# Performance work log

Measured on AMD Instinct MI355X. Metric: run time of the kernel, lower is better.

The kernel has to match this reference:

```python
import jax, jax.numpy as jnp
import numpy as np

N_QUBITS = 14
N_LAYERS = 4
N_CLASSES = 10
BATCH = 1024


def apply_1q(state, gate, wire):
    """Apply a 2x2 gate ([2,2] shared or [B,2,2] batched) to `wire` of state [B,2,...,2]."""
    s = jnp.moveaxis(state, wire + 1, -1)
    shp = s.shape
    s = s.reshape(shp[0], -1, 2)
    if gate.ndim == 3:
        s = jnp.einsum('bij,bkj->bki', gate, s)
    else:
        s = jnp.einsum('ij,bkj->bki', gate, s)
    return jnp.moveaxis(s.reshape(shp), -1, wire + 1)


def apply_cnot(state, c, t):
    s = jnp.moveaxis(state, (c + 1, t + 1), (-2, -1))
    s = jnp.stack([s[..., 0, :], s[..., 1, ::-1]], axis=-2)
    return jnp.moveaxis(s, (-2, -1), (c + 1, t + 1))


def simulate(x, q_params):
    """Batched statevector sim of: RY(x_i) embed -> BasicEntanglerLayers(RX + CNOT ring) -> <Z_i>."""
    B, n = x.shape
    state = jnp.zeros((B,) + (2,) * n, jnp.complex64)
    state = state.at[(slice(None),) + (0,) * n].set(1.0)

    # RY(x_i) on each wire (angles batched per sample)
    c, s = jnp.cos(0.5 * x), jnp.sin(0.5 * x)
    for w in range(n):
        g = jnp.stack([jnp.stack([c[:, w], -s[:, w]], -1),
                       jnp.stack([s[:, w], c[:, w]], -1)], -2).astype(jnp.complex64)  # [B,2,2]
        state = apply_1q(state, g, w)

    # BasicEntanglerLayers: per layer RX(weights[l,i]) on every wire, then CNOT ring
    cw, sw = jnp.cos(0.5 * q_params), jnp.sin(0.5 * q_params)
    n_layers = q_params.shape[0]
    for l in range(n_layers):
        for w in range(n):
            cc = cw[l, w].astype(jnp.complex64)
            isw = (-1j) * sw[l, w].astype(jnp.complex64)
            g = jnp.stack([jnp.stack([cc, isw]), jnp.stack([isw, cc])])  # [2,2] RX
            state = apply_1q(state, g, w)
        if n == 2:
            state = apply_cnot(state, 0, 1)
        else:
            for w in range(n):
                state = apply_cnot(state, w, (w + 1) % n)

    # <Z_i> = P(bit_i=0) - P(bit_i=1)
    p = jnp.abs(state) ** 2  # [B,2,...,2] real
    axes_all = tuple(range(1, n + 1))
    z = []
    for w in range(n):
        pw = jnp.sum(p, axis=tuple(a for a in axes_all if a != w + 1))  # [B,2]
        z.append(pw[:, 0] - pw[:, 1])
    return jnp.stack(z, -1).astype(jnp.float32)  # [B, n]


def setup_inputs() -> dict:
    key = jax.random.key(0)
    k1, k2, k3, k4 = jax.random.split(key, 4)
    x = jax.random.normal(k1, (BATCH, N_QUBITS), dtype=jnp.float32)
    q_params = 0.01 * jax.random.normal(k2, (N_LAYERS, N_QUBITS), dtype=jnp.float32)
    fc_w = jax.random.normal(k3, (N_CLASSES, N_QUBITS), dtype=jnp.float32) / np.sqrt(N_QUBITS)
    fc_b = jax.random.normal(k4, (N_CLASSES,), dtype=jnp.float32) * 0.01
    return {"x": x, "q_params": q_params, "fc_w": fc_w, "fc_b": fc_b}


def reference(x, q_params, fc_w, fc_b):
    q_out = simulate(x, q_params)            # [B, n_qubits]
    logits = q_out @ fc_w.T + fc_b           # [B, n_classes]
    return logits
```

## Files before the change

kernel.cpp:

```cpp
#include <hip/hip_runtime.h>
#include <hip/hip_fp16.h>
#include <math.h>


#define NQ 14
#define NSTATE (1 << NQ)
#define NLAYERS 4
#define NCLASSES 10
#define BLOCK 512
#define PADN (NSTATE + (NSTATE >> 5))

template<int LO, int M, int STEP, bool IS_RX, bool INIT, int PRE_CTRL, int POST_CTRL, bool CHAIN, bool FINAL>
__device__ __forceinline__ void run_pass(__half2* __restrict__ st,
                                         const __half2* __restrict__ cw,
                                         const __half2* __restrict__ sw,
                                         float* __restrict__ zloc)
{
  constexpr int KN  = 1 << M;
  constexpr int NCH = NSTATE >> M;
  __half2 c[M], s[M];
#pragma unroll
  for (int j = 0; j < M; ++j) { c[j] = cw[j]; s[j] = sw[j]; }

  for (int chunk = threadIdx.x; chunk < NCH; chunk += BLOCK) {
    const int low   = chunk & ((1 << LO) - 1);
    const int high  = chunk >> LO;
    const int base  = low | (high << (LO + M));
    const int pbase = base + (base >> 5);
    __half2 a[KN];
    if constexpr (INIT) {
#pragma unroll
      for (int k = 0; k < KN; ++k) a[k] = __floats2half2_rn(0.f, 0.f);
      if (chunk == 0) a[0] = __floats2half2_rn(1.f, 0.f);
    } else {
#pragma unroll
      for (int k = 0; k < KN; ++k) a[k] = st[pbase + k * STEP];
    }
    if constexpr (PRE_CTRL >= 0) {
      if ((base >> PRE_CTRL) & 1) {
#pragma unroll
        for (int k = 0; k < KN; k += 2) { __half2 t = a[k]; a[k] = a[k + 1]; a[k + 1] = t; }
      }
    }
#pragma unroll
    for (int j = 0; j < M; ++j) {
#pragma unroll
      for (int k = 0; k < KN; ++k) {
        if ((k & (1 << j)) == 0) {
          const int k1 = k | (1 << j);
          const __half2 a0 = a[k], a1 = a[k1];
          if constexpr (IS_RX) {
            a[k]  = __hfma2(s[j], __lowhigh2highlow(a1), __hmul2(c[j], a0));
            a[k1] = __hfma2(s[j], __lowhigh2highlow(a0), __hmul2(c[j], a1));
          } else {
            a[k]  = __hsub2(__hmul2(c[j], a0), __hmul2(s[j], a1));
            a[k1] = __hfma2(s[j], a0, __hmul2(c[j], a1));
          }
        }
      }
    }
    if constexpr (POST_CTRL >= 0) {
      if ((base >> POST_CTRL) & 1) {
#pragma unroll
        for (int k = 0; k < KN; k += 2) { __half2 t = a[k]; a[k] = a[k + 1]; a[k + 1] = t; }
      }
    }
    if constexpr (CHAIN) {
#pragma unroll
      for (int j = 0; j < M - 1; ++j) {
#pragma unroll
        for (int k = 0; k < KN; ++k) {
          if ((k & (1 << j)) != 0 && (k & (1 << (j + 1))) == 0) {
            const int k2 = k | (1 << (j + 1));
            __half2 t = a[k]; a[k] = a[k2]; a[k2] = t;
          }
        }
      }
    }
    if constexpr (FINAL) {
      float ssum = 0.f, sb0 = 0.f, sb1 = 0.f, sb2 = 0.f, sb3 = 0.f;
#pragma unroll
      for (int k = 0; k < KN; ++k) {
        const float2 v = __half22float2(a[k]);
        const float p = fmaf(v.x, v.x, v.y * v.y);
        ssum += p;
        if (k & 1) sb0 += p;
        if (k & 2) sb1 += p;
        if (k & 4) sb2 += p;
        if (k & 8) sb3 += p;
      }
      zloc[10] += ssum - 2.f * sb0;
      zloc[11] += ssum - 2.f * sb1;
      zloc[12] += ssum - 2.f * sb2;
      zloc[13] += ssum - 2.f * sb3;
      const float z0 = ssum - 2.f * sb3;
      zloc[0] += (base & 1) ? -z0 : z0;
#pragma unroll
      for (int w = 1; w < 10; ++w) zloc[w] += ((base >> w) & 1) ? -ssum : ssum;
    } else {
#pragma unroll
      for (int k = 0; k < KN; ++k) st[pbase + k * STEP] = a[k];
    }
  }
}

__global__ __launch_bounds__(BLOCK) void qsim_kernel(
    const float* __restrict__ x, const float* __restrict__ qp,
    const float* __restrict__ fcw, const float* __restrict__ fcb,
    float* __restrict__ out)
{
  extern __shared__ unsigned char smem[];
  __half2* st  = (__half2*)smem;
  __half2* ryc = st + PADN;
  __half2* rys = ryc + NQ;
  __half2* rxc = rys + NQ;
  __half2* rxs = rxc + NLAYERS * NQ;
  float*   zbuf  = (float*)(rxs + NLAYERS * NQ);
  float*   zpart = zbuf + NQ;

  const int b   = blockIdx.x;
  const int tid = threadIdx.x;

  if (tid < NQ) {
    float sv, cv;
    sincosf(0.5f * x[b * NQ + tid], &sv, &cv);
    ryc[tid] = __floats2half2_rn(cv, cv);
    rys[tid] = __floats2half2_rn(sv, sv);
  } else if (tid >= 64 && tid < 64 + NLAYERS * NQ) {
    const int k = tid - 64;
    float sv, cv;
    sincosf(0.5f * qp[k], &sv, &cv);
    rxc[k] = __floats2half2_rn(cv, cv);
    rxs[k] = __floats2half2_rn(sv, -sv);
  }
  __syncthreads();

  run_pass<0, 5, 1,    false, true,  -1, -1, false, false>(st, ryc,      rys,      nullptr); __syncthreads();
  run_pass<5, 5, 33,   false, false, -1, -1, false, false>(st, ryc + 5,  rys + 5,  nullptr); __syncthreads();
  run_pass<10, 4, 1056,false, false, -1, -1, false, false>(st, ryc + 10, rys + 10, nullptr); __syncthreads();

  float zloc[NQ];
#pragma unroll
  for (int w = 0; w < NQ; ++w) zloc[w] = 0.f;

#pragma unroll
  for (int l = 0; l < NLAYERS; ++l) {
    const __half2* lc = rxc + l * NQ;
    const __half2* ls = rxs + l * NQ;
    if (l == 0) run_pass<0, 5, 1, true, false, -1, -1, true, false>(st, lc, ls, nullptr);
    else        run_pass<0, 5, 1, true, false, 13, -1, true, false>(st, lc, ls, nullptr);
    __syncthreads();
    run_pass<5, 5, 33, true, false, -1, 4, true, false>(st, lc + 5, ls + 5, nullptr);
    __syncthreads();
    if (l < NLAYERS - 1) {
      run_pass<10, 4, 1056, true, false, -1, 9, true, false>(st, lc + 10, ls + 10, nullptr);
      __syncthreads();
    } else {
      run_pass<10, 4, 1056, true, false, -1, 9, true, true>(st, lc + 10, ls + 10, zloc);
    }
  }

#pragma unroll
  for (int w = 0; w < NQ; ++w) {
#pragma unroll
    for (int off = 32; off > 0; off >>= 1)
      zloc[w] += __shfl_down(zloc[w], off, 64);
  }
  const int wave = tid >> 6, lane = tid & 63;
  if (lane == 0) {
#pragma unroll
    for (int w = 0; w < NQ; ++w) zpart[wave * NQ + w] = zloc[w];
  }
  __syncthreads();
  if (tid < NQ) {
    float acc = 0.f;
#pragma unroll
    for (int v = 0; v < BLOCK / 64; ++v) acc += zpart[v * NQ + tid];
    zbuf[tid] = acc;
  }
  __syncthreads();

  if (tid < NCLASSES) {
    float acc = fcb[tid];
#pragma unroll
    for (int w = 0; w < NQ; ++w) acc = fmaf(zbuf[w], fcw[tid * NQ + w], acc);
    out[b * NCLASSES + tid] = acc;
  }
}

extern "C" void kernel_launch(void* const* d_in, const int* in_sizes, int n_in,
                              void* d_out, int out_size, void* d_ws, size_t ws_size,
                              hipStream_t stream) {
  const float* x   = (const float*)d_in[0];
  const float* qp  = (const float*)d_in[1];
  const float* fcw = (const float*)d_in[2];
  const float* fcb = (const float*)d_in[3];
  float* out = (float*)d_out;
  const int B = in_sizes[0] / NQ;

  const size_t shmem = (size_t)PADN * sizeof(__half2)
                     + (size_t)(2 * NQ + 2 * NLAYERS * NQ) * sizeof(__half2)
                     + (size_t)(NQ + (BLOCK / 64) * NQ) * sizeof(float);
  (void)hipFuncSetAttribute((const void*)qsim_kernel,
                            hipFuncAttributeMaxDynamicSharedMemorySize, (int)shmem);
  qsim_kernel<<<B, BLOCK, shmem, stream>>>(x, qp, fcw, fcb, out);
}
```

Measured before the change: 145.2 us.

## Restructure state passes for vectorized LDS access with wider padding

Replaces the generic templated pass with three specialized passes (A, B, C) that read and write shared-memory state using float4/float2 vector loads. The padding now inserts 4 half2 words every 32 instead of one, so 8- and 16-byte accesses stay aligned. Pass B gives each thread two adjacent amplitudes per group and runs on only 256 threads with 64 amplitudes each. The aim is fewer, wider LDS instructions with fewer bank conflicts, at the cost of higher register pressure and half the threads idle in pass B.

```diff
diff --git a/kernel.cpp b/kernel.cpp
--- a/kernel.cpp
+++ b/kernel.cpp
@@ -4,102 +4,193 @@
 
 
 #define NQ 14
-#define NSTATE (1 << NQ)
+#define NSTATE 16384
 #define NLAYERS 4
 #define NCLASSES 10
 #define BLOCK 512
-#define PADN (NSTATE + (NSTATE >> 5))
-
-template<int LO, int M, int STEP, bool IS_RX, bool INIT, int PRE_CTRL, int POST_CTRL, bool CHAIN, bool FINAL>
-__device__ __forceinline__ void run_pass(__half2* __restrict__ st,
-                                         const __half2* __restrict__ cw,
-                                         const __half2* __restrict__ sw,
-                                         float* __restrict__ zloc)
-{
-  constexpr int KN  = 1 << M;
-  constexpr int NCH = NSTATE >> M;
-  __half2 c[M], s[M];
-#pragma unroll
-  for (int j = 0; j < M; ++j) { c[j] = cw[j]; s[j] = sw[j]; }
-
-  for (int chunk = threadIdx.x; chunk < NCH; chunk += BLOCK) {
-    const int low   = chunk & ((1 << LO) - 1);
-    const int high  = chunk >> LO;
-    const int base  = low | (high << (LO + M));
-    const int pbase = base + (base >> 5);
-    __half2 a[KN];
-    if constexpr (INIT) {
-#pragma unroll
-      for (int k = 0; k < KN; ++k) a[k] = __floats2half2_rn(0.f, 0.f);
-      if (chunk == 0) a[0] = __floats2half2_rn(1.f, 0.f);
-    } else {
-#pragma unroll
-      for (int k = 0; k < KN; ++k) a[k] = st[pbase + k * STEP];
-    }
-    if constexpr (PRE_CTRL >= 0) {
-      if ((base >> PRE_CTRL) & 1) {
-#pragma unroll
-        for (int k = 0; k < KN; k += 2) { __half2 t = a[k]; a[k] = a[k + 1]; a[k + 1] = t; }
-      }
-    }
-#pragma unroll
-    for (int j = 0; j < M; ++j) {
-#pragma unroll
-      for (int k = 0; k < KN; ++k) {
-        if ((k & (1 << j)) == 0) {
-          const int k1 = k | (1 << j);
-          const __half2 a0 = a[k], a1 = a[k1];
-          if constexpr (IS_RX) {
-            a[k]  = __hfma2(s[j], __lowhigh2highlow(a1), __hmul2(c[j], a0));
-            a[k1] = __hfma2(s[j], __lowhigh2highlow(a0), __hmul2(c[j], a1));
-          } else {
-            a[k]  = __hsub2(__hmul2(c[j], a0), __hmul2(s[j], a1));
-            a[k1] = __hfma2(s[j], a0, __hmul2(c[j], a1));
-          }
+#define PADN (NSTATE + ((NSTATE >> 5) << 2))
+
+__device__ __forceinline__ int pidx(int i) { return i + ((i >> 5) << 2); }
+__device__ __forceinline__ __half2 f2h(float f) { return __builtin_bit_cast(__half2, f); }
+__device__ __forceinline__ float   h2f(__half2 h) { return __builtin_bit_cast(float, h); }
+
+template<bool IS_RX>
+__device__ __forceinline__ void rot_pair(__half2& a0r, __half2& a1r,
+                                         const __half2 cj, const __half2 sj,
+                                         const __half2 nsj)
+{
+  const __half2 a0 = a0r, a1 = a1r;
+  if constexpr (IS_RX) {
+    a0r = __hfma2(sj, __lowhigh2highlow(a1), __hmul2(cj, a0));
+    a1r = __hfma2(sj, __lowhigh2highlow(a0), __hmul2(cj, a1));
+  } else {
+    a0r = __hfma2(nsj, a1, __hmul2(cj, a0));
+    a1r = __hfma2(sj,  a0, __hmul2(cj, a1));
+  }
+}
+
+template<bool IS_RX, bool INIT, bool PRE_WRAP, bool CHAIN>
+__device__ __forceinline__ void pass_A(__half2* __restrict__ st,
+                                       const __half2* __restrict__ cw,
+                                       const __half2* __restrict__ sw)
+{
+  __half2 c[5], s[5];
+#pragma unroll
+  for (int j = 0; j < 5; ++j) { c[j] = cw[j]; s[j] = sw[j]; }
+  const int ch = threadIdx.x;
+  float4* base = (float4*)(st + 36 * ch);
+  __half2 a[32];
+  if constexpr (INIT) {
+#pragma unroll
+    for (int k = 0; k < 32; ++k) a[k] = f2h(0.f);
+    if (ch == 0) a[0] = __floats2half2_rn(1.f, 0.f);
+  } else {
+#pragma unroll
+    for (int m = 0; m < 8; ++m) {
+      const float4 v = base[m];
+      a[4*m+0] = f2h(v.x); a[4*m+1] = f2h(v.y);
+      a[4*m+2] = f2h(v.z); a[4*m+3] = f2h(v.w);
+    }
+  }
+  if constexpr (PRE_WRAP) {
+    if ((ch >> 8) & 1) {
+#pragma unroll
+      for (int k = 0; k < 32; k += 2) { __half2 t = a[k]; a[k] = a[k+1]; a[k+1] = t; }
+    }
+  }
+#pragma unroll
+  for (int j = 0; j < 5; ++j) {
+    const __half2 cj = c[j], sj = s[j], nsj = __hneg2(s[j]);
+#pragma unroll
+    for (int k = 0; k < 32; ++k)
+      if ((k & (1 << j)) == 0) rot_pair<IS_RX>(a[k], a[k | (1 << j)], cj, sj, nsj);
+  }
+  if constexpr (CHAIN) {
+#pragma unroll
+    for (int j = 0; j < 4; ++j)
+#pragma unroll
+      for (int k = 0; k < 32; ++k)
+        if ((k & (1 << j)) != 0 && (k & (2 << j)) == 0) {
+          const int k2 = k | (2 << j);
+          __half2 t = a[k]; a[k] = a[k2]; a[k2] = t;
         }
-      }
-    }
-    if constexpr (POST_CTRL >= 0) {
-      if ((base >> POST_CTRL) & 1) {
-#pragma unroll
-        for (int k = 0; k < KN; k += 2) { __half2 t = a[k]; a[k] = a[k + 1]; a[k + 1] = t; }
-      }
-    }
-    if constexpr (CHAIN) {
-#pragma unroll
-      for (int j = 0; j < M - 1; ++j) {
-#pragma unroll
-        for (int k = 0; k < KN; ++k) {
-          if ((k & (1 << j)) != 0 && (k & (1 << (j + 1))) == 0) {
-            const int k2 = k | (1 << (j + 1));
-            __half2 t = a[k]; a[k] = a[k2]; a[k2] = t;
-          }
+  }
+#pragma unroll
+  for (int m = 0; m < 8; ++m) {
+    float4 v;
+    v.x = h2f(a[4*m+0]); v.y = h2f(a[4*m+1]);
+    v.z = h2f(a[4*m+2]); v.w = h2f(a[4*m+3]);
+    base[m] = v;
+  }
+}
+
+template<bool IS_RX, bool DO_CNOT>
+__device__ __forceinline__ void pass_B(__half2* __restrict__ st,
+                                       const __half2* __restrict__ cw,
+                                       const __half2* __restrict__ sw)
+{
+  __half2 c[5], s[5];
+#pragma unroll
+  for (int j = 0; j < 5; ++j) { c[j] = cw[j]; s[j] = sw[j]; }
+  const int ch = threadIdx.x;
+  __half2* bp = st + pidx(((ch & 15) << 1) | ((ch >> 4) << 10));
+  __half2 a[64];
+#pragma unroll
+  for (int g = 0; g < 32; ++g) {
+    const float2 v = *(const float2*)(bp + 36 * g);
+    a[2*g] = f2h(v.x); a[2*g+1] = f2h(v.y);
+  }
+#pragma unroll
+  for (int j = 0; j < 5; ++j) {
+    const __half2 cj = c[j], sj = s[j], nsj = __hneg2(s[j]);
+#pragma unroll
+    for (int r = 0; r < 64; ++r)
+      if ((r & (2 << j)) == 0) rot_pair<IS_RX>(a[r], a[r | (2 << j)], cj, sj, nsj);
+  }
+  if constexpr (DO_CNOT) {
+    if ((ch >> 3) & 1) {
+#pragma unroll
+      for (int r = 0; r < 64; ++r)
+        if ((r & 2) == 0) { const int r1 = r | 2; __half2 t = a[r]; a[r] = a[r1]; a[r1] = t; }
+    }
+#pragma unroll
+    for (int j = 0; j < 4; ++j)
+#pragma unroll
+      for (int r = 0; r < 64; ++r)
+        if ((r & (2 << j)) != 0 && (r & (4 << j)) == 0) {
+          const int r2 = r | (4 << j);
+          __half2 t = a[r]; a[r] = a[r2]; a[r2] = t;
         }
-      }
-    }
-    if constexpr (FINAL) {
-      float ssum = 0.f, sb0 = 0.f, sb1 = 0.f, sb2 = 0.f, sb3 = 0.f;
-#pragma unroll
-      for (int k = 0; k < KN; ++k) {
-        const float2 v = __half22float2(a[k]);
-        const float p = fmaf(v.x, v.x, v.y * v.y);
-        ssum += p;
-        if (k & 1) sb0 += p;
-        if (k & 2) sb1 += p;
-        if (k & 4) sb2 += p;
-        if (k & 8) sb3 += p;
-      }
-      zloc[10] += ssum - 2.f * sb0;
-      zloc[11] += ssum - 2.f * sb1;
-      zloc[12] += ssum - 2.f * sb2;
-      zloc[13] += ssum - 2.f * sb3;
-      const float z0 = ssum - 2.f * sb3;
-      zloc[0] += (base & 1) ? -z0 : z0;
-#pragma unroll
-      for (int w = 1; w < 10; ++w) zloc[w] += ((base >> w) & 1) ? -ssum : ssum;
-    } else {
-#pragma unroll
-      for (int k = 0; k < KN; ++k) st[pbase + k * STEP] = a[k];
+  }
+#pragma unroll
+  for (int g = 0; g < 32; ++g) {
+    float2 v; v.x = h2f(a[2*g]); v.y = h2f(a[2*g+1]);
+    *(float2*)(bp + 36 * g) = v;
+  }
+}
+
+template<bool IS_RX, bool DO_CNOT, bool FINAL>
+__device__ __forceinline__ void pass_C(__half2* __restrict__ st,
+                                       const __half2* __restrict__ cw,
+                                       const __half2* __restrict__ sw,
+                                       float* __restrict__ zloc)
+{
+  __half2 c[4], s[4];
+#pragma unroll
+  for (int j = 0; j < 4; ++j) { c[j] = cw[j]; s[j] = sw[j]; }
+  const int ch = threadIdx.x;
+  __half2* bp = st + pidx(ch << 1);
+  __half2 a[32];
+#pragma unroll
+  for (int h = 0; h < 16; ++h) {
+    const float2 v = *(const float2*)(bp + 1152 * h);
+    a[2*h] = f2h(v.x); a[2*h+1] = f2h(v.y);
+  }
+#pragma unroll
+  for (int j = 0; j < 4; ++j) {
+    const __half2 cj = c[j], sj = s[j], nsj = __hneg2(s[j]);
+#pragma unroll
+    for (int r = 0; r < 32; ++r)
+      if ((r & (2 << j)) == 0) rot_pair<IS_RX>(a[r], a[r | (2 << j)], cj, sj, nsj);
+  }
+  if constexpr (DO_CNOT) {
+    if ((ch >> 8) & 1) {
+#pragma unroll
+      for (int r = 0; r < 32; ++r)
+        if ((r & 2) == 0) { const int r1 = r | 2; __half2 t = a[r]; a[r] = a[r1]; a[r1] = t; }
+    }
+#pragma unroll
+    for (int j = 0; j < 3; ++j)
+#pragma unroll
+      for (int r = 0; r < 32; ++r)
+        if ((r & (2 << j)) != 0 && (r & (4 << j)) == 0) {
+          const int r2 = r | (4 << j);
+          __half2 t = a[r]; a[r] = a[r2]; a[r2] = t;
+        }
+  }
+  if constexpr (FINAL) {
+    float ssum = 0.f, sx0 = 0.f, sb[4] = {0.f, 0.f, 0.f, 0.f};
+#pragma unroll
+    for (int r = 0; r < 32; ++r) {
+      const float2 v = __half22float2(a[r]);
+      const float p = fmaf(v.x, v.x, v.y * v.y);
+      ssum += p;
+      if ((r ^ (r >> 4)) & 1) sx0 += p;
+      if (r & 2)  sb[0] += p;
+      if (r & 4)  sb[1] += p;
+      if (r & 8)  sb[2] += p;
+      if (r & 16) sb[3] += p;
+    }
+    zloc[0] += ssum - 2.f * sx0;
+#pragma unroll
+    for (int j = 0; j < 4; ++j) zloc[10 + j] += ssum - 2.f * sb[j];
+#pragma unroll
+    for (int w = 1; w <= 9; ++w) zloc[w] += ((ch >> (w - 1)) & 1) ? -ssum : ssum;
+  } else {
+#pragma unroll
+    for (int h = 0; h < 16; ++h) {
+      float2 v; v.x = h2f(a[2*h]); v.y = h2f(a[2*h+1]);
+      *(float2*)(bp + 1152 * h) = v;
     }
   }
 }
@@ -135,9 +226,9 @@
   }
   __syncthreads();
 
-  run_pass<0, 5, 1,    false, true,  -1, -1, false, false>(st, ryc,      rys,      nullptr); __syncthreads();
-  run_pass<5, 5, 33,   false, false, -1, -1, false, false>(st, ryc + 5,  rys + 5,  nullptr); __syncthreads();
-  run_pass<10, 4, 1056,false, false, -1, -1, false, false>(st, ryc + 10, rys + 10, nullptr); __syncthreads();
+  pass_A<false, true, false, false>(st, ryc, rys);            __syncthreads();
+  if (tid < 256) pass_B<false, false>(st, ryc + 5, rys + 5);  __syncthreads();
+  pass_C<false, false, false>(st, ryc + 10, rys + 10, nullptr); __syncthreads();
 
   float zloc[NQ];
 #pragma unroll
@@ -147,16 +238,16 @@
   for (int l = 0; l < NLAYERS; ++l) {
     const __half2* lc = rxc + l * NQ;
     const __half2* ls = rxs + l * NQ;
-    if (l == 0) run_pass<0, 5, 1, true, false, -1, -1, true, false>(st, lc, ls, nullptr);
-    else        run_pass<0, 5, 1, true, false, 13, -1, true, false>(st, lc, ls, nullptr);
+    if (l == 0) pass_A<true, false, false, true>(st, lc, ls);
+    else        pass_A<true, false, true,  true>(st, lc, ls);
     __syncthreads();
-    run_pass<5, 5, 33, true, false, -1, 4, true, false>(st, lc + 5, ls + 5, nullptr);
+    if (tid < 256) pass_B<true, true>(st, lc + 5, ls + 5);
     __syncthreads();
     if (l < NLAYERS - 1) {
-      run_pass<10, 4, 1056, true, false, -1, 9, true, false>(st, lc + 10, ls + 10, nullptr);
+      pass_C<true, true, false>(st, lc + 10, ls + 10, nullptr);
       __syncthreads();
     } else {
-      run_pass<10, 4, 1056, true, false, -1, 9, true, true>(st, lc + 10, ls + 10, zloc);
+      pass_C<true, true, true>(st, lc + 10, ls + 10, zloc);
     }
   }
 
```

Result: slower. 172.6 us (+18.8%).

## Pack amplitudes as split real/imag half2 pairs with one-chunk-per-thread passes

Applied to the files above, without the earlier changes.

Changes the shared-memory state layout so that each half2 word holds two amplitudes' real parts (and a separate word holds their imaginary parts), loaded with float2 vector accesses. The three passes are rewritten so each thread handles exactly one 16-pair chunk. The wire in the packed half2 is rotated within the word or across lanes via xor-1 shuffles. CNOT chains are folded into index remapping and lane shuffles. It also adds an occupancy hint to launch bounds, aiming to halve shared-memory traffic per gate and cut loop and indexing overhead, at the cost of more complex indexing and extra shuffles.

```diff
diff --git a/kernel.cpp b/kernel.cpp
--- a/kernel.cpp
+++ b/kernel.cpp
@@ -4,121 +4,254 @@
 
 
 #define NQ 14
-#define NSTATE (1 << NQ)
 #define NLAYERS 4
 #define NCLASSES 10
 #define BLOCK 512
-#define PADN (NSTATE + (NSTATE >> 5))
-
-template<int LO, int M, int STEP, bool IS_RX, bool INIT, int PRE_CTRL, int POST_CTRL, bool CHAIN, bool FINAL>
-__device__ __forceinline__ void run_pass(__half2* __restrict__ st,
-                                         const __half2* __restrict__ cw,
-                                         const __half2* __restrict__ sw,
-                                         float* __restrict__ zloc)
-{
-  constexpr int KN  = 1 << M;
-  constexpr int NCH = NSTATE >> M;
-  __half2 c[M], s[M];
-#pragma unroll
-  for (int j = 0; j < M; ++j) { c[j] = cw[j]; s[j] = sw[j]; }
-
-  for (int chunk = threadIdx.x; chunk < NCH; chunk += BLOCK) {
-    const int low   = chunk & ((1 << LO) - 1);
-    const int high  = chunk >> LO;
-    const int base  = low | (high << (LO + M));
-    const int pbase = base + (base >> 5);
-    __half2 a[KN];
-    if constexpr (INIT) {
-#pragma unroll
-      for (int k = 0; k < KN; ++k) a[k] = __floats2half2_rn(0.f, 0.f);
-      if (chunk == 0) a[0] = __floats2half2_rn(1.f, 0.f);
+#define NWORDS 16384
+#define PADW (NWORDS + ((NWORDS >> 6) << 1))
+
+__device__ __forceinline__ __half2 bch(unsigned u) { return __builtin_bit_cast(__half2, u); }
+__device__ __forceinline__ unsigned hcb(__half2 v) { return __builtin_bit_cast(unsigned, v); }
+__device__ __forceinline__ __half2 hswap(__half2 v) { return __lowhigh2highlow(v); }
+__device__ __forceinline__ __half2 shfl1(__half2 v) {
+  return __builtin_bit_cast(__half2, __shfl_xor(__builtin_bit_cast(float, v), 1, 64));
+}
+__host__ __device__ constexpr int chainmap(int k) {
+  int p = k ^ (((k >> 2) & 1) << 3);
+  p ^= (((p >> 1) & 1) << 2);
+  p ^= ((p & 1) << 1);
+  return p;
+}
+
+template<bool IS_RX>
+__device__ __forceinline__ void rot_regs(__half2* rev, __half2* imv, int k, int k1,
+                                         __half2 c2, __half2 s2, __half2 ns2) {
+  const __half2 r0 = rev[k], m0 = imv[k], r1 = rev[k1], m1 = imv[k1];
+  if constexpr (IS_RX) {
+    rev[k]  = __hfma2(s2, m1, __hmul2(c2, r0));
+    imv[k]  = __hfma2(ns2, r1, __hmul2(c2, m0));
+    rev[k1] = __hfma2(s2, m0, __hmul2(c2, r1));
+    imv[k1] = __hfma2(ns2, r0, __hmul2(c2, m1));
+  } else {
+    rev[k]  = __hfma2(ns2, r1, __hmul2(c2, r0));
+    imv[k]  = __hfma2(ns2, m1, __hmul2(c2, m0));
+    rev[k1] = __hfma2(s2, r0, __hmul2(c2, r1));
+    imv[k1] = __hfma2(s2, m0, __hmul2(c2, m1));
+  }
+}
+
+template<bool IS_RX, bool INIT, bool WRAP, bool CHAIN>
+__device__ __forceinline__ void pass_A(__half2* __restrict__ st,
+                                       const __half2* __restrict__ cw,
+                                       const __half2* __restrict__ sw) {
+  const int ch = threadIdx.x;
+  __half2* bp = st + 32 * ch + 2 * (ch >> 1);
+  __half2 rev[16], imv[16];
+  if constexpr (INIT) {
+#pragma unroll
+    for (int k = 0; k < 16; ++k) { rev[k] = bch(0u); imv[k] = bch(0u); }
+    if (ch == 0) rev[0] = __floats2half2_rn(1.f, 0.f);
+  } else {
+#pragma unroll
+    for (int k = 0; k < 16; ++k) {
+      const float2 v = *(const float2*)(bp + 2 * k);
+      rev[k] = __builtin_bit_cast(__half2, v.x);
+      imv[k] = __builtin_bit_cast(__half2, v.y);
+    }
+  }
+  if constexpr (WRAP) {
+    if ((ch >> 8) & 1) {
+#pragma unroll
+      for (int k = 0; k < 16; ++k) { rev[k] = hswap(rev[k]); imv[k] = hswap(imv[k]); }
+    }
+  }
+  {
+    const __half2 c2 = cw[0], s2 = sw[0];
+    if constexpr (IS_RX) {
+      const __half2 ns2 = __hneg2(s2);
+#pragma unroll
+      for (int k = 0; k < 16; ++k) {
+        const __half2 orv = rev[k], omv = imv[k];
+        rev[k] = __hfma2(s2, hswap(omv), __hmul2(c2, orv));
+        imv[k] = __hfma2(ns2, hswap(orv), __hmul2(c2, omv));
+      }
     } else {
-#pragma unroll
-      for (int k = 0; k < KN; ++k) a[k] = st[pbase + k * STEP];
-    }
-    if constexpr (PRE_CTRL >= 0) {
-      if ((base >> PRE_CTRL) & 1) {
-#pragma unroll
-        for (int k = 0; k < KN; k += 2) { __half2 t = a[k]; a[k] = a[k + 1]; a[k + 1] = t; }
-      }
-    }
-#pragma unroll
-    for (int j = 0; j < M; ++j) {
-#pragma unroll
-      for (int k = 0; k < KN; ++k) {
-        if ((k & (1 << j)) == 0) {
-          const int k1 = k | (1 << j);
-          const __half2 a0 = a[k], a1 = a[k1];
-          if constexpr (IS_RX) {
-            a[k]  = __hfma2(s[j], __lowhigh2highlow(a1), __hmul2(c[j], a0));
-            a[k1] = __hfma2(s[j], __lowhigh2highlow(a0), __hmul2(c[j], a1));
-          } else {
-            a[k]  = __hsub2(__hmul2(c[j], a0), __hmul2(s[j], a1));
-            a[k1] = __hfma2(s[j], a0, __hmul2(c[j], a1));
-          }
-        }
-      }
-    }
-    if constexpr (POST_CTRL >= 0) {
-      if ((base >> POST_CTRL) & 1) {
-#pragma unroll
-        for (int k = 0; k < KN; k += 2) { __half2 t = a[k]; a[k] = a[k + 1]; a[k + 1] = t; }
-      }
-    }
-    if constexpr (CHAIN) {
-#pragma unroll
-      for (int j = 0; j < M - 1; ++j) {
-#pragma unroll
-        for (int k = 0; k < KN; ++k) {
-          if ((k & (1 << j)) != 0 && (k & (1 << (j + 1))) == 0) {
-            const int k2 = k | (1 << (j + 1));
-            __half2 t = a[k]; a[k] = a[k2]; a[k2] = t;
-          }
-        }
-      }
-    }
-    if constexpr (FINAL) {
-      float ssum = 0.f, sb0 = 0.f, sb1 = 0.f, sb2 = 0.f, sb3 = 0.f;
-#pragma unroll
-      for (int k = 0; k < KN; ++k) {
-        const float2 v = __half22float2(a[k]);
-        const float p = fmaf(v.x, v.x, v.y * v.y);
-        ssum += p;
-        if (k & 1) sb0 += p;
-        if (k & 2) sb1 += p;
-        if (k & 4) sb2 += p;
-        if (k & 8) sb3 += p;
-      }
-      zloc[10] += ssum - 2.f * sb0;
-      zloc[11] += ssum - 2.f * sb1;
-      zloc[12] += ssum - 2.f * sb2;
-      zloc[13] += ssum - 2.f * sb3;
-      const float z0 = ssum - 2.f * sb3;
-      zloc[0] += (base & 1) ? -z0 : z0;
-#pragma unroll
-      for (int w = 1; w < 10; ++w) zloc[w] += ((base >> w) & 1) ? -ssum : ssum;
+      const __half2 mix = bch(hcb(s2) ^ 0x8000u);
+#pragma unroll
+      for (int k = 0; k < 16; ++k) {
+        rev[k] = __hfma2(mix, hswap(rev[k]), __hmul2(c2, rev[k]));
+        imv[k] = __hfma2(mix, hswap(imv[k]), __hmul2(c2, imv[k]));
+      }
+    }
+  }
+#pragma unroll
+  for (int j = 0; j < 4; ++j) {
+    const __half2 c2 = cw[1 + j], s2 = sw[1 + j], ns2 = __hneg2(sw[1 + j]);
+#pragma unroll
+    for (int k = 0; k < 16; ++k)
+      if ((k & (1 << j)) == 0) rot_regs<IS_RX>(rev, imv, k, k | (1 << j), c2, s2, ns2);
+  }
+  if constexpr (CHAIN) {
+#pragma unroll
+    for (int k = 0; k < 16; k += 2) {
+      const unsigned ra = hcb(rev[k]), rb = hcb(rev[k + 1]);
+      rev[k]     = bch((ra & 0xFFFFu) | (rb & 0xFFFF0000u));
+      rev[k + 1] = bch((rb & 0xFFFFu) | (ra & 0xFFFF0000u));
+      const unsigned ma = hcb(imv[k]), mb = hcb(imv[k + 1]);
+      imv[k]     = bch((ma & 0xFFFFu) | (mb & 0xFFFF0000u));
+      imv[k + 1] = bch((mb & 0xFFFFu) | (ma & 0xFFFF0000u));
+    }
+  }
+#pragma unroll
+  for (int k = 0; k < 16; ++k) {
+    const int src = CHAIN ? chainmap(k) : k;
+    float2 v;
+    v.x = __builtin_bit_cast(float, rev[src]);
+    v.y = __builtin_bit_cast(float, imv[src]);
+    *(float2*)(bp + 2 * k) = v;
+  }
+}
+
+template<bool IS_RX, bool CNOTS>
+__device__ __forceinline__ void pass_B(__half2* __restrict__ st,
+                                       const __half2* __restrict__ cw,
+                                       const __half2* __restrict__ sw) {
+  const int ch = threadIdx.x;
+  const int u = ((ch >> 1) & 15) | ((ch & 1) << 8) | ((ch >> 5) << 9);
+  __half2* bp = st + 2 * u + 2 * (u >> 5);
+  __half2 rev[16], imv[16];
+#pragma unroll
+  for (int k = 0; k < 16; ++k) {
+    const float2 v = *(const float2*)(bp + 32 * k + 2 * (k >> 1));
+    rev[k] = __builtin_bit_cast(__half2, v.x);
+    imv[k] = __builtin_bit_cast(__half2, v.y);
+  }
+#pragma unroll
+  for (int j = 0; j < 4; ++j) {
+    const __half2 c2 = cw[j], s2 = sw[j], ns2 = __hneg2(sw[j]);
+#pragma unroll
+    for (int k = 0; k < 16; ++k)
+      if ((k & (1 << j)) == 0) rot_regs<IS_RX>(rev, imv, k, k | (1 << j), c2, s2, ns2);
+  }
+  {
+    const __half2 c2 = cw[4], s2 = sw[4];
+    if constexpr (IS_RX) {
+      const __half2 ns2 = __hneg2(s2);
+#pragma unroll
+      for (int k = 0; k < 16; ++k) {
+        const __half2 pr = shfl1(rev[k]), pm = shfl1(imv[k]);
+        rev[k] = __hfma2(s2, pm, __hmul2(c2, rev[k]));
+        imv[k] = __hfma2(ns2, pr, __hmul2(c2, imv[k]));
+      }
     } else {
-#pragma unroll
-      for (int k = 0; k < KN; ++k) st[pbase + k * STEP] = a[k];
-    }
-  }
-}
-
-__global__ __launch_bounds__(BLOCK) void qsim_kernel(
+      const __half2 sg = (ch & 1) ? s2 : __hneg2(s2);
+#pragma unroll
+      for (int k = 0; k < 16; ++k) {
+        const __half2 pr = shfl1(rev[k]), pm = shfl1(imv[k]);
+        rev[k] = __hfma2(sg, pr, __hmul2(c2, rev[k]));
+        imv[k] = __hfma2(sg, pm, __hmul2(c2, imv[k]));
+      }
+    }
+  }
+  if constexpr (CNOTS) {
+    if ((ch >> 4) & 1) {
+#pragma unroll
+      for (int k = 0; k < 16; k += 2) {
+        __half2 t = rev[k]; rev[k] = rev[k + 1]; rev[k + 1] = t;
+        t = imv[k]; imv[k] = imv[k + 1]; imv[k + 1] = t;
+      }
+    }
+  }
+#pragma unroll
+  for (int k = 0; k < 16; ++k) {
+    const int src = CNOTS ? chainmap(k) : k;
+    __half2 vr = rev[src], vm = imv[src];
+    if constexpr (CNOTS) {
+      if (k & 8) { vr = shfl1(vr); vm = shfl1(vm); }
+    }
+    float2 v;
+    v.x = __builtin_bit_cast(float, vr);
+    v.y = __builtin_bit_cast(float, vm);
+    *(float2*)(bp + 32 * k + 2 * (k >> 1)) = v;
+  }
+}
+
+template<bool IS_RX, bool CNOTS, bool FINAL>
+__device__ __forceinline__ void pass_C(__half2* __restrict__ st,
+                                       const __half2* __restrict__ cw,
+                                       const __half2* __restrict__ sw,
+                                       float* __restrict__ zloc) {
+  const int ch = threadIdx.x;
+  __half2* bp = st + 2 * ch + 2 * (ch >> 5);
+  __half2 rev[16], imv[16];
+#pragma unroll
+  for (int k = 0; k < 16; ++k) {
+    const float2 v = *(const float2*)(bp + 1056 * k);
+    rev[k] = __builtin_bit_cast(__half2, v.x);
+    imv[k] = __builtin_bit_cast(__half2, v.y);
+  }
+#pragma unroll
+  for (int j = 0; j < 4; ++j) {
+    const __half2 c2 = cw[j], s2 = sw[j], ns2 = __hneg2(sw[j]);
+#pragma unroll
+    for (int k = 0; k < 16; ++k)
+      if ((k & (1 << j)) == 0) rot_regs<IS_RX>(rev, imv, k, k | (1 << j), c2, s2, ns2);
+  }
+  if constexpr (CNOTS) {
+    if ((ch >> 8) & 1) {
+#pragma unroll
+      for (int k = 0; k < 16; k += 2) {
+        __half2 t = rev[k]; rev[k] = rev[k + 1]; rev[k + 1] = t;
+        t = imv[k]; imv[k] = imv[k + 1]; imv[k + 1] = t;
+      }
+    }
+  }
+  if constexpr (FINAL) {
+    float ssum = 0.f, z0 = 0.f, zA = 0.f, zB = 0.f, zC = 0.f, zD = 0.f;
+#pragma unroll
+    for (int k = 0; k < 16; ++k) {
+      const int src = chainmap(k);
+      const float2 r = __half22float2(rev[src]);
+      const float2 m = __half22float2(imv[src]);
+      const float p0 = fmaf(r.x, r.x, m.x * m.x);
+      const float p1 = fmaf(r.y, r.y, m.y * m.y);
+      const float ps = p0 + p1, d = p0 - p1;
+      ssum += ps;
+      z0 += (k & 8) ? -d : d;
+      zA += (k & 1) ? -ps : ps;
+      zB += (k & 2) ? -ps : ps;
+      zC += (k & 4) ? -ps : ps;
+      zD += (k & 8) ? -ps : ps;
+    }
+    zloc[0] = z0; zloc[10] = zA; zloc[11] = zB; zloc[12] = zC; zloc[13] = zD;
+#pragma unroll
+    for (int w = 1; w <= 9; ++w) zloc[w] = ((ch >> (w - 1)) & 1) ? -ssum : ssum;
+  } else {
+#pragma unroll
+    for (int k = 0; k < 16; ++k) {
+      const int src = CNOTS ? chainmap(k) : k;
+      float2 v;
+      v.x = __builtin_bit_cast(float, rev[src]);
+      v.y = __builtin_bit_cast(float, imv[src]);
+      *(float2*)(bp + 1056 * k) = v;
+    }
+  }
+}
+
+__global__ __launch_bounds__(BLOCK, 4) void qsim_kernel(
     const float* __restrict__ x, const float* __restrict__ qp,
     const float* __restrict__ fcw, const float* __restrict__ fcb,
-    float* __restrict__ out)
-{
+    float* __restrict__ out) {
   extern __shared__ unsigned char smem[];
   __half2* st  = (__half2*)smem;
-  __half2* ryc = st + PADN;
+  __half2* ryc = st + PADW;
   __half2* rys = ryc + NQ;
   __half2* rxc = rys + NQ;
   __half2* rxs = rxc + NLAYERS * NQ;
-  float*   zbuf  = (float*)(rxs + NLAYERS * NQ);
-  float*   zpart = zbuf + NQ;
-
-  const int b   = blockIdx.x;
+  float* zbuf  = (float*)(rxs + NLAYERS * NQ);
+  float* zpart = zbuf + NQ;
+
+  const int b = blockIdx.x;
   const int tid = threadIdx.x;
 
   if (tid < NQ) {
@@ -131,32 +264,27 @@
     float sv, cv;
     sincosf(0.5f * qp[k], &sv, &cv);
     rxc[k] = __floats2half2_rn(cv, cv);
-    rxs[k] = __floats2half2_rn(sv, -sv);
+    rxs[k] = __floats2half2_rn(sv, sv);
   }
   __syncthreads();
 
-  run_pass<0, 5, 1,    false, true,  -1, -1, false, false>(st, ryc,      rys,      nullptr); __syncthreads();
-  run_pass<5, 5, 33,   false, false, -1, -1, false, false>(st, ryc + 5,  rys + 5,  nullptr); __syncthreads();
-  run_pass<10, 4, 1056,false, false, -1, -1, false, false>(st, ryc + 10, rys + 10, nullptr); __syncthreads();
+  pass_A<false, true, false, false>(st, ryc, rys);             __syncthreads();
+  pass_B<false, false>(st, ryc + 5, rys + 5);                  __syncthreads();
+  pass_C<false, false, false>(st, ryc + 10, rys + 10, nullptr); __syncthreads();
 
   float zloc[NQ];
-#pragma unroll
-  for (int w = 0; w < NQ; ++w) zloc[w] = 0.f;
-
 #pragma unroll
   for (int l = 0; l < NLAYERS; ++l) {
     const __half2* lc = rxc + l * NQ;
     const __half2* ls = rxs + l * NQ;
-    if (l == 0) run_pass<0, 5, 1, true, false, -1, -1, true, false>(st, lc, ls, nullptr);
-    else        run_pass<0, 5, 1, true, false, 13, -1, true, false>(st, lc, ls, nullptr);
+    if (l == 0) pass_A<true, false, false, true>(st, lc, ls);
+    else        pass_A<true, false, true, true>(st, lc, ls);
     __syncthreads();
-    run_pass<5, 5, 33, true, false, -1, 4, true, false>(st, lc + 5, ls + 5, nullptr);
-    __syncthreads();
+    pass_B<true, true>(st, lc + 5, ls + 5);                    __syncthreads();
     if (l < NLAYERS - 1) {
-      run_pass<10, 4, 1056, true, false, -1, 9, true, false>(st, lc + 10, ls + 10, nullptr);
-      __syncthreads();
+      pass_C<true, true, false>(st, lc + 10, ls + 10, nullptr); __syncthreads();
     } else {
-      run_pass<10, 4, 1056, true, false, -1, 9, true, true>(st, lc + 10, ls + 10, zloc);
+      pass_C<true, true, true>(st, lc + 10, ls + 10, zloc);
     }
   }
 
@@ -198,7 +326,7 @@
   float* out = (float*)d_out;
   const int B = in_sizes[0] / NQ;
 
-  const size_t shmem = (size_t)PADN * sizeof(__half2)
+  const size_t shmem = (size_t)PADW * sizeof(__half2)
                      + (size_t)(2 * NQ + 2 * NLAYERS * NQ) * sizeof(__half2)
                      + (size_t)(NQ + (BLOCK / 64) * NQ) * sizeof(float);
   (void)hipFuncSetAttribute((const void*)qsim_kernel,
```

Result: slower. 161.6 us (+11.3%).
